# Kernel tuning notes

Measured on AMD Instinct MI355X. Metric: run time of the kernel, lower is better.

The kernel has to match this reference:

```python
import jax, jax.numpy as jnp
import numpy as np

B, S, H, E, V = 128, 400, 256, 128, 50000
PAD = 250  # extended-vocab padding hard-coded in the torch module


def setup_inputs() -> dict:
    key = jax.random.key(0)
    ks = jax.random.split(key, 20)
    return {
        "input_token": jax.random.randint(ks[0], (B, 1), 0, V),
        "last_decoder_hidden": jax.random.normal(ks[1], (B, H), jnp.float32),
        "encoder_states": jax.random.normal(ks[2], (B, S, H), jnp.float32),
        "full_input_var": jax.random.randint(ks[3], (B, S), 0, V + PAD),
        "emb_table": jax.random.normal(ks[4], (V, E), jnp.float32) * 0.02,
        "gru_w_ih": jax.random.normal(ks[5], (3 * H, E), jnp.float32) * 0.05,
        "gru_w_hh": jax.random.normal(ks[6], (3 * H, H), jnp.float32) * 0.05,
        "gru_b_ih": jax.random.normal(ks[7], (3 * H,), jnp.float32) * 0.05,
        "gru_b_hh": jax.random.normal(ks[8], (3 * H,), jnp.float32) * 0.05,
        "w_h": jax.random.normal(ks[9], (H,), jnp.float32),
        "w_s": jax.random.normal(ks[10], (H,), jnp.float32),
        "att_bias": jax.random.normal(ks[11], (1,), jnp.float32),
        "attn_v": jax.random.normal(ks[12], (H,), jnp.float32),
        "gen_w": jax.random.normal(ks[13], (1, 2 * H + E), jnp.float32) * 0.05,
        "gen_b": jax.random.normal(ks[14], (1,), jnp.float32) * 0.05,
        "outh_w": jax.random.normal(ks[15], (E, 2 * H), jnp.float32) * 0.05,
        "outh_b": jax.random.normal(ks[16], (E,), jnp.float32) * 0.05,
        "outv_w": jax.random.normal(ks[17], (V, E), jnp.float32) * 0.05,
        "outv_b": jax.random.normal(ks[18], (V,), jnp.float32) * 0.05,
    }


def reference(input_token, last_decoder_hidden, encoder_states, full_input_var,
              emb_table, gru_w_ih, gru_w_hh, gru_b_ih, gru_b_hh,
              w_h, w_s, att_bias, attn_v, gen_w, gen_b,
              outh_w, outh_b, outv_w, outv_b):
    b, s, h = encoder_states.shape
    v = outv_w.shape[0]
    # Embedding lookup (dropout is identity in eval mode): [B, E]
    x = emb_table[input_token[:, 0]]
    # Single-step GRU cell (PyTorch gate order: r, z, n)
    gi = x @ gru_w_ih.T + gru_b_ih
    gh = last_decoder_hidden @ gru_w_hh.T + gru_b_hh
    i_r, i_z, i_n = jnp.split(gi, 3, axis=-1)
    h_r, h_z, h_n = jnp.split(gh, 3, axis=-1)
    r = jax.nn.sigmoid(i_r + h_r)
    z = jax.nn.sigmoid(i_z + h_z)
    n = jnp.tanh(i_n + r * h_n)
    h_new = (1.0 - z) * n + z * last_decoder_hidden  # [B, H]
    # Bahdanau-style elementwise attention
    att = jnp.tanh(w_h * encoder_states + w_s * h_new[:, None, :] + att_bias)  # [B,S,H]
    scores = jnp.einsum('bsh,h->bs', att, attn_v)
    att_dist = jax.nn.softmax(scores, axis=-1)  # [B, S]
    context = jnp.einsum('bs,bsh->bh', att_dist, encoder_states)  # [B, H]
    dec_ctx = jnp.concatenate([h_new, context], axis=-1)  # [B, 2H]
    p_vocab = jax.nn.softmax((dec_ctx @ outh_w.T + outh_b) @ outv_w.T + outv_b, axis=-1)  # [B, V]
    p_gen = jax.nn.sigmoid(jnp.concatenate([dec_ctx, x], axis=1) @ gen_w.T + gen_b)  # [B, 1]
    # Pointer scatter-add into extended vocab [B, V+PAD]
    rows = jnp.arange(b)[:, None]
    token_input_dist = jnp.zeros((b, v + PAD), p_vocab.dtype).at[rows, full_input_var].add(att_dist)
    p_final = jnp.concatenate([p_vocab * p_gen, jnp.zeros((b, PAD), p_vocab.dtype)], axis=1) \
              + (1.0 - p_gen) * token_input_dist
    return (h_new, p_final, p_gen, p_vocab, att_dist)
```

## Files before the change

### kernel.cpp

```cpp
#include <hip/hip_runtime.h>
#include <hip/hip_bf16.h>


#define B_ 128
#define S_ 400
#define H_ 256
#define E_ 128
#define V_ 50000
#define PAD_ 250
#define VP_ (V_ + PAD_)
#define NSUM_ 16

typedef unsigned short ushort_t;
typedef __attribute__((ext_vector_type(8))) short bf16x8;
typedef __attribute__((ext_vector_type(4))) float f32x4;

__device__ __forceinline__ unsigned short f2bfu(float f) {
    __hip_bfloat16 h = __float2bfloat16(f);
    union { __hip_bfloat16 h; unsigned short u; } c;
    c.h = h;
    return c.u;
}

__device__ __forceinline__ float sigmoid_fast(float x) {
    return 1.0f / (1.0f + __expf(-x));
}

__device__ __forceinline__ float tanh_fast(float x) {
    return 1.0f - 2.0f / (__expf(2.0f * x) + 1.0f);
}

__device__ __forceinline__ float waveReduceSumAll(float v) {
#pragma unroll
    for (int off = 1; off < 64; off <<= 1) v += __shfl_xor(v, off, 64);
    return v;
}

__global__ __launch_bounds__(256) void k_gates(
    const int* __restrict__ token, const float* __restrict__ emb,
    const float* __restrict__ hprev,
    const float* __restrict__ w_ih, const float* __restrict__ w_hh,
    float* __restrict__ gi_ws, float* __restrict__ gh_ws) {
    __shared__ ushort_t xh[B_ * 264];
    __shared__ int toks[B_];
    int t = threadIdx.x;
    bool isIH = blockIdx.x < 12;
    if (isIH) {
        if (t < B_) toks[t] = token[t];
        __syncthreads();
#pragma unroll
        for (int i = 0; i < 16; i++) {
            int fidx = i * 256 + t;
            int b = fidx >> 5, k4 = fidx & 31;
            float4 q = *(const float4*)(emb + (size_t)toks[b] * E_ + k4 * 4);
            ushort4 u;
            u.x = f2bfu(q.x); u.y = f2bfu(q.y); u.z = f2bfu(q.z); u.w = f2bfu(q.w);
            *(ushort4*)&xh[b * 136 + k4 * 4] = u;
        }
    } else {
#pragma unroll
        for (int i = 0; i < 32; i++) {
            int fidx = i * 256 + t;
            int b = fidx >> 6, k4 = fidx & 63;
            float4 q = *(const float4*)(hprev + (size_t)b * H_ + k4 * 4);
            ushort4 u;
            u.x = f2bfu(q.x); u.y = f2bfu(q.y); u.z = f2bfu(q.z); u.w = f2bfu(q.w);
            *(ushort4*)&xh[b * 264 + k4 * 4] = u;
        }
    }
    __syncthreads();

    int wave = t >> 6, lane = t & 63, lm = lane & 15, quad = lane >> 4;
    int tile = (isIH ? blockIdx.x : blockIdx.x - 12) * 4 + wave;
    int v = tile * 16 + lm;
    int K = isIH ? E_ : H_;
    int pitch = isIH ? 136 : 264;
    const float* wrow = (isIH ? w_ih : w_hh) + (size_t)v * K;
    float* gout = isIH ? gi_ws : gh_ws;

    f32x4 acc[8];
#pragma unroll
    for (int bt = 0; bt < 8; bt++) acc[bt] = (f32x4){0.f, 0.f, 0.f, 0.f};

    for (int kc = 0; kc < (K >> 5); kc++) {
        int k0 = kc * 32 + quad * 8;
        float4 w0 = *(const float4*)(wrow + k0);
        float4 w1 = *(const float4*)(wrow + k0 + 4);
        bf16x8 bf;
        bf[0] = (short)f2bfu(w0.x); bf[1] = (short)f2bfu(w0.y);
        bf[2] = (short)f2bfu(w0.z); bf[3] = (short)f2bfu(w0.w);
        bf[4] = (short)f2bfu(w1.x); bf[5] = (short)f2bfu(w1.y);
        bf[6] = (short)f2bfu(w1.z); bf[7] = (short)f2bfu(w1.w);
#pragma unroll
        for (int bt = 0; bt < 8; bt++) {
            bf16x8 af = *(const bf16x8*)&xh[(bt * 16 + lm) * pitch + k0];
            acc[bt] = __builtin_amdgcn_mfma_f32_16x16x32_bf16(af, bf, acc[bt], 0, 0, 0);
        }
    }
#pragma unroll
    for (int bt = 0; bt < 8; bt++)
#pragma unroll
        for (int r = 0; r < 4; r++) {
            int b = bt * 16 + quad * 4 + r;
            gout[(size_t)b * 768 + v] = acc[bt][r];
        }
}

__global__ __launch_bounds__(1024) void k_attn_combine(
    const float* __restrict__ gi_ws, const float* __restrict__ gh_ws,
    const float* __restrict__ b_ih, const float* __restrict__ b_hh,
    const float* __restrict__ hprev,
    const float* __restrict__ enc,
    const float* __restrict__ w_h, const float* __restrict__ w_s,
    const float* __restrict__ att_bias, const float* __restrict__ attn_v,
    const int* __restrict__ token, const float* __restrict__ emb,
    const float* __restrict__ outh_w, const float* __restrict__ outh_b,
    const float* __restrict__ gen_w, const float* __restrict__ gen_b,
    float* __restrict__ out_hnew, float* __restrict__ out_attd,
    float* __restrict__ out_pgen,
    float* __restrict__ hidden_ws, float* __restrict__ row_sum16) {
    int b = blockIdx.x;
    int t = threadIdx.x;
    int wave = t >> 6, lane = t & 63;
    __shared__ float whs[H_], vs[H_], cs[H_], cmerge[H_];
    __shared__ float scl[S_];
    __shared__ float mred[16], lred[16], r2[16];
    __shared__ float dc[2 * H_ + E_];

    if (b == 0) {
        for (int i = t; i < NSUM_ * B_; i += 1024) row_sum16[i] = 0.0f;
    }
    if (t < H_) {
        float ir = gi_ws[(size_t)b * 768 + t] + b_ih[t];
        float iz = gi_ws[(size_t)b * 768 + 256 + t] + b_ih[256 + t];
        float in_ = gi_ws[(size_t)b * 768 + 512 + t] + b_ih[512 + t];
        float hr = gh_ws[(size_t)b * 768 + t] + b_hh[t];
        float hz = gh_ws[(size_t)b * 768 + 256 + t] + b_hh[256 + t];
        float hn = gh_ws[(size_t)b * 768 + 512 + t] + b_hh[512 + t];
        float hp = hprev[(size_t)b * H_ + t];
        float r = sigmoid_fast(ir + hr);
        float z = sigmoid_fast(iz + hz);
        float n = tanh_fast(in_ + r * hn);
        float h = (1.0f - z) * n + z * hp;
        out_hnew[(size_t)b * H_ + t] = h;
        dc[t] = h;
        whs[t] = w_h[t];
        vs[t] = attn_v[t];
        cs[t] = w_s[t] * h + att_bias[0];
        cmerge[t] = 0.0f;
    }
    if (t < E_) dc[2 * H_ + t] = emb[(size_t)token[b] * E_ + t];
    __syncthreads();

    int h0 = lane * 4;
    float wh0 = whs[h0], wh1 = whs[h0 + 1], wh2 = whs[h0 + 2], wh3 = whs[h0 + 3];
    float vv0 = vs[h0], vv1 = vs[h0 + 1], vv2 = vs[h0 + 2], vv3 = vs[h0 + 3];
    float cc0 = cs[h0], cc1 = cs[h0 + 1], cc2 = cs[h0 + 2], cc3 = cs[h0 + 3];

    float m_w = -1e30f, l_w = 0.0f;
    float cx0 = 0.f, cx1 = 0.f, cx2 = 0.f, cx3 = 0.f;
    for (int s = wave; s < S_; s += 16) {
        float4 u = *(const float4*)(enc + ((size_t)(b * S_ + s)) * H_ + h0);
        float p = vv0 * tanh_fast(wh0 * u.x + cc0)
                + vv1 * tanh_fast(wh1 * u.y + cc1)
                + vv2 * tanh_fast(wh2 * u.z + cc2)
                + vv3 * tanh_fast(wh3 * u.w + cc3);
        p = waveReduceSumAll(p);
        if (lane == 0) scl[s] = p;
        float mn = fmaxf(m_w, p);
        float scale = __expf(m_w - mn);
        float w = __expf(p - mn);
        cx0 = cx0 * scale + w * u.x;
        cx1 = cx1 * scale + w * u.y;
        cx2 = cx2 * scale + w * u.z;
        cx3 = cx3 * scale + w * u.w;
        l_w = l_w * scale + w;
        m_w = mn;
    }
    if (lane == 0) mred[wave] = m_w;
    __syncthreads();
    float M = -1e30f;
#pragma unroll
    for (int i = 0; i < 16; i++) M = fmaxf(M, mred[i]);
    float wf = __expf(m_w - M);
    if (lane == 0) lred[wave] = l_w * wf;
    atomicAdd(&cmerge[h0 + 0], cx0 * wf);
    atomicAdd(&cmerge[h0 + 1], cx1 * wf);
    atomicAdd(&cmerge[h0 + 2], cx2 * wf);
    atomicAdd(&cmerge[h0 + 3], cx3 * wf);
    __syncthreads();
    float L = 0.0f;
#pragma unroll
    for (int i = 0; i < 16; i++) L += lred[i];
    float invL = 1.0f / L;

    for (int s = t; s < S_; s += 1024) {
        out_attd[(size_t)b * S_ + s] = __expf(scl[s] - M) * invL;
    }
    if (t < H_) dc[H_ + t] = cmerge[t] * invL;
    __syncthreads();

    {
        int r = t >> 3, sub = t & 7;
        const float* wrow = outh_w + (size_t)r * (2 * H_);
        float acc = 0.0f;
#pragma unroll
        for (int i = 0; i < 16; i++) {
            int k = i * 32 + sub * 4;
            float4 q = *(const float4*)(wrow + k);
            acc += dc[k] * q.x + dc[k + 1] * q.y + dc[k + 2] * q.z + dc[k + 3] * q.w;
        }
        acc += __shfl_down(acc, 4, 64);
        acc += __shfl_down(acc, 2, 64);
        acc += __shfl_down(acc, 1, 64);
        if (sub == 0) hidden_ws[(size_t)b * E_ + r] = acc + outh_b[r];
    }
    float pp = (t < 2 * H_ + E_) ? dc[t] * gen_w[t] : 0.0f;
    pp = waveReduceSumAll(pp);
    if (lane == 0) r2[wave] = pp;
    __syncthreads();
    if (t == 0) {
        float g = 0.0f;
#pragma unroll
        for (int wv = 0; wv < 16; wv++) g += r2[wv];
        out_pgen[b] = sigmoid_fast(g + gen_b[0]);
    }
}

#define VT_TOTAL (V_ / 16)
#define HID_PITCH 136
__global__ __launch_bounds__(256) void k_vocab_mfma(
    const float* __restrict__ outv_w, const float* __restrict__ outv_b,
    const float* __restrict__ hidden_ws,
    float* __restrict__ out_pvocab, float* __restrict__ row_sum16) {
    __shared__ ushort_t hid[B_ * HID_PITCH];
    __shared__ float rsum[B_];
    int t = threadIdx.x;

    const float4* h4 = (const float4*)hidden_ws;
#pragma unroll
    for (int i = 0; i < 16; i++) {
        int fidx = i * 256 + t;
        float4 q = h4[fidx];
        int row = fidx >> 5;
        int col = (fidx & 31) << 2;
        ushort4 u;
        u.x = f2bfu(q.x); u.y = f2bfu(q.y); u.z = f2bfu(q.z); u.w = f2bfu(q.w);
        *(ushort4*)&hid[row * HID_PITCH + col] = u;
    }
    if (t < B_) rsum[t] = 0.0f;
    __syncthreads();

    int wave = t >> 6, lane = t & 63, lm = lane & 15, quad = lane >> 4;
    int vt = blockIdx.x * 4 + wave;

    if (vt < VT_TOTAL) {
        int v = vt * 16 + lm;
        const float* wrow = outv_w + (size_t)v * E_;

        f32x4 acc[8];
#pragma unroll
        for (int bt = 0; bt < 8; bt++) acc[bt] = (f32x4){0.f, 0.f, 0.f, 0.f};

#pragma unroll
        for (int kc = 0; kc < 4; kc++) {
            int k0 = kc * 32 + quad * 8;
            float4 w0 = *(const float4*)(wrow + k0);
            float4 w1 = *(const float4*)(wrow + k0 + 4);
            bf16x8 bf;
            bf[0] = (short)f2bfu(w0.x); bf[1] = (short)f2bfu(w0.y);
            bf[2] = (short)f2bfu(w0.z); bf[3] = (short)f2bfu(w0.w);
            bf[4] = (short)f2bfu(w1.x); bf[5] = (short)f2bfu(w1.y);
            bf[6] = (short)f2bfu(w1.z); bf[7] = (short)f2bfu(w1.w);
#pragma unroll
            for (int bt = 0; bt < 8; bt++) {
                bf16x8 af = *(const bf16x8*)&hid[(bt * 16 + lm) * HID_PITCH + k0];
                acc[bt] = __builtin_amdgcn_mfma_f32_16x16x32_bf16(af, bf, acc[bt], 0, 0, 0);
            }
        }

        float bias = outv_b[v];
#pragma unroll
        for (int bt = 0; bt < 8; bt++) {
#pragma unroll
            for (int r = 0; r < 4; r++) {
                int b = bt * 16 + quad * 4 + r;
                float e = __expf(fminf(acc[bt][r] + bias, 60.0f));
                out_pvocab[(size_t)b * V_ + v] = e;
                float s = e;
                s += __shfl_xor(s, 1);
                s += __shfl_xor(s, 2);
                s += __shfl_xor(s, 4);
                s += __shfl_xor(s, 8);
                if (lm == 0) atomicAdd(&rsum[b], s);
            }
        }
    }
    __syncthreads();
    if (t < B_) atomicAdd(&row_sum16[(blockIdx.x & (NSUM_ - 1)) * B_ + t], rsum[t]);
}

__global__ __launch_bounds__(1024) void k_final_scatter(
    const float* __restrict__ row_sum16, const float* __restrict__ pgen,
    const int* __restrict__ fiv, const float* __restrict__ attd,
    float* __restrict__ out_pfinal, float* __restrict__ out_pvocab) {
    int b = blockIdx.x;
    int t = threadIdx.x;
    float rs = 0.0f;
#pragma unroll
    for (int i = 0; i < NSUM_; i++) rs += row_sum16[i * B_ + b];
    float inv = 1.0f / rs;
    float pg = pgen[b];
    float omg = 1.0f - pg;
    float* pvrow = out_pvocab + (size_t)b * V_;
    float* pfrow = out_pfinal + (size_t)b * VP_;

    for (int i4 = t; i4 < V_ / 4; i4 += 1024) {
        float4 p = *(float4*)(pvrow + i4 * 4);
        p.x *= inv; p.y *= inv; p.z *= inv; p.w *= inv;
        *(float4*)(pvrow + i4 * 4) = p;
        float2 a; a.x = p.x * pg; a.y = p.y * pg;
        float2 c; c.x = p.z * pg; c.y = p.w * pg;
        *(float2*)(pfrow + i4 * 4) = a;
        *(float2*)(pfrow + i4 * 4 + 2) = c;
    }
    if (t < PAD_) pfrow[V_ + t] = 0.0f;
    __syncthreads();
    if (t < S_) {
        int idx = fiv[b * S_ + t];
        atomicAdd(&pfrow[idx], omg * attd[(size_t)b * S_ + t]);
    }
}

extern "C" void kernel_launch(void* const* d_in, const int* in_sizes, int n_in,
                              void* d_out, int out_size, void* d_ws, size_t ws_size,
                              hipStream_t stream) {
    const int* token = (const int*)d_in[0];
    const float* hprev = (const float*)d_in[1];
    const float* enc = (const float*)d_in[2];
    const int* fiv = (const int*)d_in[3];
    const float* emb = (const float*)d_in[4];
    const float* w_ih = (const float*)d_in[5];
    const float* w_hh = (const float*)d_in[6];
    const float* b_ih = (const float*)d_in[7];
    const float* b_hh = (const float*)d_in[8];
    const float* w_h = (const float*)d_in[9];
    const float* w_s = (const float*)d_in[10];
    const float* att_bias = (const float*)d_in[11];
    const float* attn_v = (const float*)d_in[12];
    const float* gen_w = (const float*)d_in[13];
    const float* gen_b = (const float*)d_in[14];
    const float* outh_w = (const float*)d_in[15];
    const float* outh_b = (const float*)d_in[16];
    const float* outv_w = (const float*)d_in[17];
    const float* outv_b = (const float*)d_in[18];

    float* out = (float*)d_out;
    float* out_hnew = out;
    float* out_pfinal = out + (size_t)B_ * H_;
    float* out_pgen = out_pfinal + (size_t)B_ * VP_;
    float* out_pvocab = out_pgen + B_;
    float* out_attd = out_pvocab + (size_t)B_ * V_;

    float* wsf = (float*)d_ws;
    float* gi_ws = wsf;
    float* gh_ws = wsf + 98304;
    float* hidden_ws = wsf + 196608;
    float* row_sum16 = wsf + 212992;

    k_gates<<<24, 256, 0, stream>>>(token, emb, hprev, w_ih, w_hh, gi_ws, gh_ws);
    k_attn_combine<<<B_, 1024, 0, stream>>>(gi_ws, gh_ws, b_ih, b_hh, hprev,
                                            enc, w_h, w_s, att_bias, attn_v,
                                            token, emb, outh_w, outh_b, gen_w, gen_b,
                                            out_hnew, out_attd, out_pgen,
                                            hidden_ws, row_sum16);
    k_vocab_mfma<<<782, 256, 0, stream>>>(outv_w, outv_b, hidden_ws, out_pvocab, row_sum16);
    k_final_scatter<<<B_, 1024, 0, stream>>>(row_sum16, out_pgen, fiv, out_attd,
                                             out_pfinal, out_pvocab);
}
```

Measured before the change: 233.2 us.

## Split attention and final scatter across multiple blocks per row with last-block merge

Attention now runs on 8 blocks of 256 threads per batch row, each covering a 50-position chunk of the sequence. Each block writes its partial max, sum and context to workspace, and the last block to finish (found with an atomic counter) merges them and computes the output projection and p_gen. The final normalise/scatter kernel is likewise split into 25 blocks per row, with the last block doing the pointer scatter-add. The aim is more blocks and better occupancy on the GPU. The cost is extra workspace traffic, atomic counters and thread fences, and counter resets moved into the gates kernel.

```diff
diff --git a/kernel.cpp b/kernel.cpp
--- a/kernel.cpp
+++ b/kernel.cpp
@@ -9,7 +9,10 @@
 #define V_ 50000
 #define PAD_ 250
 #define VP_ (V_ + PAD_)
+#define NC_ 8
+#define CS_ (S_ / NC_)
 #define NSUM_ 16
+#define GF_ 25
 
 typedef unsigned short ushort_t;
 typedef __attribute__((ext_vector_type(8))) short bf16x8;
@@ -40,11 +43,16 @@
     const int* __restrict__ token, const float* __restrict__ emb,
     const float* __restrict__ hprev,
     const float* __restrict__ w_ih, const float* __restrict__ w_hh,
-    float* __restrict__ gi_ws, float* __restrict__ gh_ws) {
+    float* __restrict__ gi_ws, float* __restrict__ gh_ws,
+    float* __restrict__ row_sum16, int* __restrict__ cnt_attn, int* __restrict__ cnt_fin) {
     __shared__ ushort_t xh[B_ * 264];
     __shared__ int toks[B_];
     int t = threadIdx.x;
     bool isIH = blockIdx.x < 12;
+    if (blockIdx.x == 0) {
+        for (int i = t; i < NSUM_ * B_; i += 256) row_sum16[i] = 0.0f;
+        if (t < B_) { cnt_attn[t] = 0; cnt_fin[t] = 0; }
+    }
     if (isIH) {
         if (t < B_) toks[t] = token[t];
         __syncthreads();
@@ -106,7 +114,7 @@
         }
 }
 
-__global__ __launch_bounds__(1024) void k_attn_combine(
+__global__ __launch_bounds__(256) void k_attn(
     const float* __restrict__ gi_ws, const float* __restrict__ gh_ws,
     const float* __restrict__ b_ih, const float* __restrict__ b_hh,
     const float* __restrict__ hprev,
@@ -118,19 +126,18 @@
     const float* __restrict__ gen_w, const float* __restrict__ gen_b,
     float* __restrict__ out_hnew, float* __restrict__ out_attd,
     float* __restrict__ out_pgen,
-    float* __restrict__ hidden_ws, float* __restrict__ row_sum16) {
-    int b = blockIdx.x;
+    float* __restrict__ sc_ws, float* __restrict__ ml_ws, float* __restrict__ ctxp_ws,
+    float* __restrict__ hidden_ws, int* __restrict__ cnt_attn) {
+    int c = blockIdx.x, b = blockIdx.y;
     int t = threadIdx.x;
     int wave = t >> 6, lane = t & 63;
-    __shared__ float whs[H_], vs[H_], cs[H_], cmerge[H_];
-    __shared__ float scl[S_];
-    __shared__ float mred[16], lred[16], r2[16];
+    __shared__ float whs[H_], vs[H_], cs[H_], cmerge[H_], hs[H_];
+    __shared__ float mred[4], lred[4], r2[4];
     __shared__ float dc[2 * H_ + E_];
-
-    if (b == 0) {
-        for (int i = t; i < NSUM_ * B_; i += 1024) row_sum16[i] = 0.0f;
-    }
-    if (t < H_) {
+    __shared__ float ml[NC_ * 2];
+    __shared__ int lastflag;
+
+    {
         float ir = gi_ws[(size_t)b * 768 + t] + b_ih[t];
         float iz = gi_ws[(size_t)b * 768 + 256 + t] + b_ih[256 + t];
         float in_ = gi_ws[(size_t)b * 768 + 512 + t] + b_ih[512 + t];
@@ -142,31 +149,27 @@
         float z = sigmoid_fast(iz + hz);
         float n = tanh_fast(in_ + r * hn);
         float h = (1.0f - z) * n + z * hp;
-        out_hnew[(size_t)b * H_ + t] = h;
-        dc[t] = h;
+        if (c == 0) out_hnew[(size_t)b * H_ + t] = h;
+        hs[t] = h;
         whs[t] = w_h[t];
         vs[t] = attn_v[t];
         cs[t] = w_s[t] * h + att_bias[0];
         cmerge[t] = 0.0f;
     }
-    if (t < E_) dc[2 * H_ + t] = emb[(size_t)token[b] * E_ + t];
     __syncthreads();
 
     int h0 = lane * 4;
-    float wh0 = whs[h0], wh1 = whs[h0 + 1], wh2 = whs[h0 + 2], wh3 = whs[h0 + 3];
-    float vv0 = vs[h0], vv1 = vs[h0 + 1], vv2 = vs[h0 + 2], vv3 = vs[h0 + 3];
-    float cc0 = cs[h0], cc1 = cs[h0 + 1], cc2 = cs[h0 + 2], cc3 = cs[h0 + 3];
-
     float m_w = -1e30f, l_w = 0.0f;
     float cx0 = 0.f, cx1 = 0.f, cx2 = 0.f, cx3 = 0.f;
-    for (int s = wave; s < S_; s += 16) {
+    for (int si = wave; si < CS_; si += 4) {
+        int s = c * CS_ + si;
         float4 u = *(const float4*)(enc + ((size_t)(b * S_ + s)) * H_ + h0);
-        float p = vv0 * tanh_fast(wh0 * u.x + cc0)
-                + vv1 * tanh_fast(wh1 * u.y + cc1)
-                + vv2 * tanh_fast(wh2 * u.z + cc2)
-                + vv3 * tanh_fast(wh3 * u.w + cc3);
+        float p = vs[h0 + 0] * tanh_fast(whs[h0 + 0] * u.x + cs[h0 + 0])
+                + vs[h0 + 1] * tanh_fast(whs[h0 + 1] * u.y + cs[h0 + 1])
+                + vs[h0 + 2] * tanh_fast(whs[h0 + 2] * u.z + cs[h0 + 2])
+                + vs[h0 + 3] * tanh_fast(whs[h0 + 3] * u.w + cs[h0 + 3]);
         p = waveReduceSumAll(p);
-        if (lane == 0) scl[s] = p;
+        if (lane == 0) sc_ws[b * S_ + s] = p;
         float mn = fmaxf(m_w, p);
         float scale = __expf(m_w - mn);
         float w = __expf(p - mn);
@@ -179,51 +182,72 @@
     }
     if (lane == 0) mred[wave] = m_w;
     __syncthreads();
-    float M = -1e30f;
-#pragma unroll
-    for (int i = 0; i < 16; i++) M = fmaxf(M, mred[i]);
-    float wf = __expf(m_w - M);
+    float m_c = fmaxf(fmaxf(mred[0], mred[1]), fmaxf(mred[2], mred[3]));
+    float wf = __expf(m_w - m_c);
     if (lane == 0) lred[wave] = l_w * wf;
     atomicAdd(&cmerge[h0 + 0], cx0 * wf);
     atomicAdd(&cmerge[h0 + 1], cx1 * wf);
     atomicAdd(&cmerge[h0 + 2], cx2 * wf);
     atomicAdd(&cmerge[h0 + 3], cx3 * wf);
     __syncthreads();
+    if (t == 0) {
+        ml_ws[(b * NC_ + c) * 2 + 0] = m_c;
+        ml_ws[(b * NC_ + c) * 2 + 1] = lred[0] + lred[1] + lred[2] + lred[3];
+    }
+    ctxp_ws[(size_t)(b * NC_ + c) * H_ + t] = cmerge[t];
+
+    __threadfence();
+    __syncthreads();
+    if (t == 0) lastflag = (atomicAdd(&cnt_attn[b], 1) == NC_ - 1);
+    __syncthreads();
+    if (!lastflag) return;
+    __threadfence();
+
+    if (t < NC_ * 2) ml[t] = ml_ws[b * NC_ * 2 + t];
+    __syncthreads();
+    float M = -1e30f;
+#pragma unroll
+    for (int cc = 0; cc < NC_; cc++) M = fmaxf(M, ml[2 * cc]);
     float L = 0.0f;
 #pragma unroll
-    for (int i = 0; i < 16; i++) L += lred[i];
+    for (int cc = 0; cc < NC_; cc++) L += ml[2 * cc + 1] * __expf(ml[2 * cc] - M);
     float invL = 1.0f / L;
 
-    for (int s = t; s < S_; s += 1024) {
-        out_attd[(size_t)b * S_ + s] = __expf(scl[s] - M) * invL;
-    }
-    if (t < H_) dc[H_ + t] = cmerge[t] * invL;
-    __syncthreads();
+    for (int s = t; s < S_; s += 256)
+        out_attd[(size_t)b * S_ + s] = __expf(sc_ws[b * S_ + s] - M) * invL;
 
     {
-        int r = t >> 3, sub = t & 7;
+        float acc = 0.0f;
+#pragma unroll
+        for (int cc = 0; cc < NC_; cc++)
+            acc += __expf(ml[2 * cc] - M) * ctxp_ws[(size_t)(b * NC_ + cc) * H_ + t];
+        dc[t] = hs[t];
+        dc[H_ + t] = acc * invL;
+    }
+    if (t < E_) dc[2 * H_ + t] = emb[(size_t)token[b] * E_ + t];
+    __syncthreads();
+
+    {
+        int r = t >> 1, sub = t & 1;
         const float* wrow = outh_w + (size_t)r * (2 * H_);
         float acc = 0.0f;
 #pragma unroll
-        for (int i = 0; i < 16; i++) {
-            int k = i * 32 + sub * 4;
+        for (int i = 0; i < 64; i++) {
+            int k = i * 8 + sub * 4;
             float4 q = *(const float4*)(wrow + k);
             acc += dc[k] * q.x + dc[k + 1] * q.y + dc[k + 2] * q.z + dc[k + 3] * q.w;
         }
-        acc += __shfl_down(acc, 4, 64);
-        acc += __shfl_down(acc, 2, 64);
         acc += __shfl_down(acc, 1, 64);
         if (sub == 0) hidden_ws[(size_t)b * E_ + r] = acc + outh_b[r];
     }
-    float pp = (t < 2 * H_ + E_) ? dc[t] * gen_w[t] : 0.0f;
-    pp = waveReduceSumAll(pp);
-    if (lane == 0) r2[wave] = pp;
-    __syncthreads();
-    if (t == 0) {
-        float g = 0.0f;
-#pragma unroll
-        for (int wv = 0; wv < 16; wv++) g += r2[wv];
-        out_pgen[b] = sigmoid_fast(g + gen_b[0]);
+    {
+        float pp = dc[t] * gen_w[t] + dc[t + 256] * gen_w[t + 256]
+                 + ((t < E_) ? dc[t + 512] * gen_w[t + 512] : 0.0f);
+        pp = waveReduceSumAll(pp);
+        if (lane == 0) r2[wave] = pp;
+        __syncthreads();
+        if (t == 0)
+            out_pgen[b] = sigmoid_fast(r2[0] + r2[1] + r2[2] + r2[3] + gen_b[0]);
     }
 }
 
@@ -300,12 +324,14 @@
     if (t < B_) atomicAdd(&row_sum16[(blockIdx.x & (NSUM_ - 1)) * B_ + t], rsum[t]);
 }
 
-__global__ __launch_bounds__(1024) void k_final_scatter(
+__global__ __launch_bounds__(256) void k_final_scatter(
     const float* __restrict__ row_sum16, const float* __restrict__ pgen,
     const int* __restrict__ fiv, const float* __restrict__ attd,
-    float* __restrict__ out_pfinal, float* __restrict__ out_pvocab) {
-    int b = blockIdx.x;
+    float* __restrict__ out_pfinal, float* __restrict__ out_pvocab,
+    int* __restrict__ cnt_fin) {
+    int g = blockIdx.x, b = blockIdx.y;
     int t = threadIdx.x;
+    __shared__ int lastflag;
     float rs = 0.0f;
 #pragma unroll
     for (int i = 0; i < NSUM_; i++) rs += row_sum16[i * B_ + b];
@@ -315,20 +341,42 @@
     float* pvrow = out_pvocab + (size_t)b * V_;
     float* pfrow = out_pfinal + (size_t)b * VP_;
 
-    for (int i4 = t; i4 < V_ / 4; i4 += 1024) {
-        float4 p = *(float4*)(pvrow + i4 * 4);
-        p.x *= inv; p.y *= inv; p.z *= inv; p.w *= inv;
-        *(float4*)(pvrow + i4 * 4) = p;
-        float2 a; a.x = p.x * pg; a.y = p.y * pg;
-        float2 c; c.x = p.z * pg; c.y = p.w * pg;
-        *(float2*)(pfrow + i4 * 4) = a;
-        *(float2*)(pfrow + i4 * 4 + 2) = c;
-    }
-    if (t < PAD_) pfrow[V_ + t] = 0.0f;
-    __syncthreads();
-    if (t < S_) {
-        int idx = fiv[b * S_ + t];
-        atomicAdd(&pfrow[idx], omg * attd[(size_t)b * S_ + t]);
+    int j0 = g * 2048;
+    for (int i4 = t; i4 < 512; i4 += 256) {
+        int j = j0 + i4 * 4;
+        if (j + 4 <= V_) {
+            float4 p = *(float4*)(pvrow + j);
+            p.x *= inv; p.y *= inv; p.z *= inv; p.w *= inv;
+            *(float4*)(pvrow + j) = p;
+            float2 a; a.x = p.x * pg; a.y = p.y * pg;
+            float2 cc; cc.x = p.z * pg; cc.y = p.w * pg;
+            *(float2*)(pfrow + j) = a;
+            *(float2*)(pfrow + j + 2) = cc;
+        } else {
+#pragma unroll
+            for (int k = 0; k < 4; k++) {
+                int jj = j + k;
+                if (jj < V_) {
+                    float p = pvrow[jj] * inv;
+                    pvrow[jj] = p;
+                    pfrow[jj] = p * pg;
+                } else if (jj < VP_) {
+                    pfrow[jj] = 0.0f;
+                }
+            }
+        }
+    }
+
+    __threadfence();
+    __syncthreads();
+    if (t == 0) lastflag = (atomicAdd(&cnt_fin[b], 1) == GF_ - 1);
+    __syncthreads();
+    if (!lastflag) return;
+    __threadfence();
+
+    for (int s = t; s < S_; s += 256) {
+        int idx = fiv[b * S_ + s];
+        atomicAdd(&pfrow[idx], omg * attd[(size_t)b * S_ + s]);
     }
 }
 
@@ -367,14 +415,21 @@
     float* gh_ws = wsf + 98304;
     float* hidden_ws = wsf + 196608;
     float* row_sum16 = wsf + 212992;
-
-    k_gates<<<24, 256, 0, stream>>>(token, emb, hprev, w_ih, w_hh, gi_ws, gh_ws);
-    k_attn_combine<<<B_, 1024, 0, stream>>>(gi_ws, gh_ws, b_ih, b_hh, hprev,
-                                            enc, w_h, w_s, att_bias, attn_v,
-                                            token, emb, outh_w, outh_b, gen_w, gen_b,
-                                            out_hnew, out_attd, out_pgen,
-                                            hidden_ws, row_sum16);
+    float* sc_ws = wsf + 215040;
+    float* ml_ws = wsf + 266240;
+    float* ctxp_ws = wsf + 268288;
+    int* cnt_attn = (int*)(wsf + 530432);
+    int* cnt_fin = (int*)(wsf + 530560);
+
+    k_gates<<<24, 256, 0, stream>>>(token, emb, hprev, w_ih, w_hh, gi_ws, gh_ws,
+                                    row_sum16, cnt_attn, cnt_fin);
+    k_attn<<<dim3(NC_, B_), 256, 0, stream>>>(gi_ws, gh_ws, b_ih, b_hh, hprev,
+                                              enc, w_h, w_s, att_bias, attn_v,
+                                              token, emb, outh_w, outh_b, gen_w, gen_b,
+                                              out_hnew, out_attd, out_pgen,
+                                              sc_ws, ml_ws, ctxp_ws,
+                                              hidden_ws, cnt_attn);
     k_vocab_mfma<<<782, 256, 0, stream>>>(outv_w, outv_b, hidden_ws, out_pvocab, row_sum16);
-    k_final_scatter<<<B_, 1024, 0, stream>>>(row_sum16, out_pgen, fiv, out_attd,
-                                             out_pfinal, out_pvocab);
-}
+    k_final_scatter<<<dim3(GF_, B_), 256, 0, stream>>>(row_sum16, out_pgen, fiv, out_attd,
+                                                       out_pfinal, out_pvocab, cnt_fin);
+}
```

Measured after the change: 713.6 us. +206.0%, slower.
